# Kernel tuning notes

Measured on AMD Instinct MI355X. Metric: run time of the kernel, lower is better.

The kernel has to match this reference:

```python
import jax, jax.numpy as jnp
import numpy as np

H, DK, DV, S = 16, 1024, 1024, 2048
DH_QK = DK // H  # 64, per-head q/k dim
DH_V = DV // H   # 64, per-head v dim


def setup_inputs() -> dict:
    key = jax.random.key(0)
    ks = jax.random.split(key, 11)
    init = lambda k, shape, fan_in: jax.random.uniform(k, shape, jnp.float32, -1.0, 1.0) / jnp.sqrt(jnp.float32(fan_in))
    return {
        "Q": jax.random.normal(ks[0], (S, DK), jnp.float32),
        "K": jax.random.normal(ks[1], (S, DK), jnp.float32),
        "V": jax.random.normal(ks[2], (S, DV), jnp.float32),
        # per-head Linear weights, torch convention [out, in] stacked over heads
        "Wq": init(ks[3], (H, DH_QK, DH_QK), DH_QK),
        "bq": init(ks[4], (H, DH_QK), DH_QK),
        "Wk": init(ks[5], (H, DH_QK, DH_QK), DH_QK),
        "bk": init(ks[6], (H, DH_QK), DH_QK),
        "Wv": init(ks[7], (H, DH_V, DH_V), DH_V),
        "bv": init(ks[8], (H, DH_V), DH_V),
        "Wo": init(ks[9], (DK, H * DH_V), H * DH_V),  # final linear: d_model x (h*dv_h)
        "bo": init(ks[10], (DK,), H * DH_V),
    }


def reference(Q, K, V, Wq, bq, Wk, bk, Wv, bv, Wo, bo):
    h, dh = Wq.shape[0], Wq.shape[2]
    dv = Wv.shape[2]
    s = Q.shape[0]
    # split features into h per-head chunks (same as slicing loop in torch)
    Qh = Q.reshape(s, h, dh)
    Kh = K.reshape(s, h, dh)
    Vh = V.reshape(s, h, dv)
    # per-head Linear: x @ W.T + b, batched over heads
    q = jnp.einsum('shd,hed->she', Qh, Wq) + bq
    k = jnp.einsum('shd,hed->she', Kh, Wk) + bk
    v = jnp.einsum('shd,hed->she', Vh, Wv) + bv
    # scaled dot-product attention per head
    scores = jnp.einsum('she,the->hst', q, k) / jnp.sqrt(jnp.float32(dh))
    attn = jax.nn.softmax(scores, axis=-1)
    o = jnp.einsum('hst,the->she', attn, v)  # [s, h, dv]
    concat = o.reshape(s, h * dv)
    return concat @ Wo.T + bo
```

## Files before the change

kernel.cpp:

```cpp
#include <hip/hip_runtime.h>
#include <stdint.h>

static constexpr int H   = 16;
static constexpr int S   = 2048;
static constexpr int DHd = 64;
static constexpr int DM  = 1024;
static constexpr int NSPLIT = 4;
static constexpr int KT_PER_SPLIT = (S / 64) / NSPLIT;

using f32x4   = __attribute__((ext_vector_type(4))) float;
using f32x8   = __attribute__((ext_vector_type(8))) float;
using f32x16  = __attribute__((ext_vector_type(16))) float;
using short8  = __attribute__((ext_vector_type(8))) short;
using bf16x8  = __attribute__((ext_vector_type(8))) __bf16;
using uint4v  = __attribute__((ext_vector_type(4))) unsigned int;

#if __has_builtin(__builtin_amdgcn_exp2f)
#define EXP2F __builtin_amdgcn_exp2f
#else
#define EXP2F exp2f
#endif

__device__ __forceinline__ short f2bf(float f) {
  union { float f; uint32_t u; } v; v.f = f;
  uint32_t r = v.u + 0x7FFFu + ((v.u >> 16) & 1u);
  return (short)(r >> 16);
}
__device__ __forceinline__ float bf2f(short s) {
  union { uint32_t u; float f; } v;
  v.u = ((uint32_t)(unsigned short)s) << 16;
  return v.f;
}

__device__ __forceinline__ short8 f2bf8(f32x4 a, f32x4 b) {
  short8 v;
  v[0] = f2bf(a[0]); v[1] = f2bf(a[1]); v[2] = f2bf(a[2]); v[3] = f2bf(a[3]);
  v[4] = f2bf(b[0]); v[5] = f2bf(b[1]); v[6] = f2bf(b[2]); v[7] = f2bf(b[3]);
  return v;
}

__device__ __forceinline__ unsigned int pkbf(float a, float b) {
  __bf16 x = (__bf16)a, y = (__bf16)b;
  unsigned short ux = __builtin_bit_cast(unsigned short, x);
  unsigned short uy = __builtin_bit_cast(unsigned short, y);
  return (unsigned int)ux | ((unsigned int)uy << 16);
}

__device__ __forceinline__ f32x4 mfma16(short8 a, short8 b, f32x4 c) {
  return __builtin_amdgcn_mfma_f32_16x16x32_bf16(
      __builtin_bit_cast(bf16x8, a), __builtin_bit_cast(bf16x8, b), c, 0, 0, 0);
}
__device__ __forceinline__ f32x16 mfma32(short8 a, short8 b, f32x16 c) {
  return __builtin_amdgcn_mfma_f32_32x32x16_bf16(
      __builtin_bit_cast(bf16x8, a), __builtin_bit_cast(bf16x8, b), c, 0, 0, 0);
}

__device__ __forceinline__ short8 lds_read_swz(const short* base, int row, int chunk) {
  return *(const short8*)((const char*)base + row * 128 + ((chunk ^ (row & 7)) << 4));
}
__device__ __forceinline__ void lds_write_swz(short* base, int row, int chunk, short8 v) {
  *(short8*)((char*)base + row * 128 + ((chunk ^ (row & 7)) << 4)) = v;
}

using u32g = __attribute__((address_space(1))) const unsigned int;
using u32l = __attribute__((address_space(3))) unsigned int;
__device__ __forceinline__ void gl_lds16(const short* g, short* l) {
  __builtin_amdgcn_global_load_lds(
      reinterpret_cast<u32g*>(reinterpret_cast<uintptr_t>(g)),
      reinterpret_cast<u32l*>(static_cast<unsigned int>(reinterpret_cast<uintptr_t>(l))),
      16, 0, 0);
}

__global__ __launch_bounds__(256) void proj_kernel(
    const float* __restrict__ Q, const float* __restrict__ K, const float* __restrict__ V,
    const float* __restrict__ Wq, const float* __restrict__ bq,
    const float* __restrict__ Wk, const float* __restrict__ bk,
    const float* __restrict__ Wv, const float* __restrict__ bv,
    const float* __restrict__ Wo, short* __restrict__ wob,
    short* __restrict__ qb, short* __restrict__ kb, short* __restrict__ vtb) {
  const int t = threadIdx.x;
  const int mode = blockIdx.z;

  if (mode == 3) {
    int chunk = blockIdx.y * gridDim.x + blockIdx.x;
    int i = (chunk * 256 + t) * 16;
    f32x4 x0 = *(const f32x4*)(Wo + i);
    f32x4 x1 = *(const f32x4*)(Wo + i + 4);
    f32x4 x2 = *(const f32x4*)(Wo + i + 8);
    f32x4 x3 = *(const f32x4*)(Wo + i + 12);
    *(short8*)(wob + i)     = f2bf8(x0, x1);
    *(short8*)(wob + i + 8) = f2bf8(x2, x3);
    return;
  }

  const int h  = blockIdx.y;
  const int rt = blockIdx.x * 128;

  const float* X; const float* W; const float* bias;
  if (mode == 0)      { X = Q; W = Wq; bias = bq; }
  else if (mode == 1) { X = K; W = Wk; bias = bk; }
  else                { X = V; W = Wv; bias = bv; }
  bias += h * DHd;
  const float scale = (mode == 0) ? 0.125f * 1.44269504f : 1.0f;

  __shared__ short Xs[128 * 64];
  __shared__ short Ws[64 * 64];
  __shared__ short Ot[64 * 136];

#pragma unroll
  for (int p = 0; p < 4; p++) {
    int ci = p * 256 + t;
    int row = ci >> 3, oct = ci & 7;
    const float* g = X + (size_t)(rt + row) * DM + h * DHd + oct * 8;
    f32x4 x0 = *(const f32x4*)g;
    f32x4 x1 = *(const f32x4*)(g + 4);
    lds_write_swz(Xs, row, oct, f2bf8(x0, x1));
  }
#pragma unroll
  for (int p = 0; p < 2; p++) {
    int ci = p * 256 + t;
    int row = ci >> 3, oct = ci & 7;
    const float* g = W + (size_t)h * DHd * DHd + row * DHd + oct * 8;
    f32x4 x0 = *(const f32x4*)g;
    f32x4 x1 = *(const f32x4*)(g + 4);
    lds_write_swz(Ws, row, oct, f2bf8(x0, x1));
  }
  __syncthreads();

  const int wid = t >> 6, lane = t & 63;
  const int l15 = lane & 15, l4 = lane >> 4;

  f32x4 acc[2][4] = {};
#pragma unroll
  for (int ks = 0; ks < 2; ks++) {
    int chunk = ks * 4 + l4;
    short8 a0 = lds_read_swz(Xs, wid * 32 + l15, chunk);
    short8 a1 = lds_read_swz(Xs, wid * 32 + 16 + l15, chunk);
#pragma unroll
    for (int nf = 0; nf < 4; nf++) {
      short8 b = lds_read_swz(Ws, nf * 16 + l15, chunk);
      acc[0][nf] = mfma16(a0, b, acc[0][nf]);
      acc[1][nf] = mfma16(a1, b, acc[1][nf]);
    }
  }

  if (mode < 2) {
    short* out = (mode == 0) ? qb : kb;
#pragma unroll
    for (int mf = 0; mf < 2; mf++)
#pragma unroll
      for (int nf = 0; nf < 4; nf++) {
        int col = nf * 16 + l15;
        float b = bias[col];
#pragma unroll
        for (int r = 0; r < 4; r++) {
          int row = rt + wid * 32 + mf * 16 + l4 * 4 + r;
          out[((size_t)h * S + row) * DHd + col] = f2bf((acc[mf][nf][r] + b) * scale);
        }
      }
  } else {
#pragma unroll
    for (int mf = 0; mf < 2; mf++)
#pragma unroll
      for (int nf = 0; nf < 4; nf++) {
        int col = nf * 16 + l15;
        float b = bias[col];
#pragma unroll
        for (int r = 0; r < 4; r++) {
          int lrow = wid * 32 + mf * 16 + l4 * 4 + r;
          Ot[col * 136 + lrow] = f2bf(acc[mf][nf][r] + b);
        }
      }
    __syncthreads();
#pragma unroll
    for (int p = 0; p < 2; p++) {
      int ci = p * 256 + t;
      int e = ci >> 3, c16 = ci & 7;
      short8 a = *(const short8*)&Ot[e * 136 + c16 * 16];
      short8 b = *(const short8*)&Ot[e * 136 + c16 * 16 + 8];
      short8 lo, hi;
      lo[0] = a[0]; lo[1] = a[1]; lo[2] = a[2]; lo[3] = a[3];
      lo[4] = b[0]; lo[5] = b[1]; lo[6] = b[2]; lo[7] = b[3];
      hi[0] = a[4]; hi[1] = a[5]; hi[2] = a[6]; hi[3] = a[7];
      hi[4] = b[4]; hi[5] = b[5]; hi[6] = b[6]; hi[7] = b[7];
      short* dst = vtb + ((size_t)h * DHd + e) * S + rt + c16 * 16;
      *(short8*)dst       = lo;
      *(short8*)(dst + 8) = hi;
    }
  }
}

__global__ __launch_bounds__(256, 2) void attn_kernel(
    const short* __restrict__ qb, const short* __restrict__ kb,
    const short* __restrict__ vtb, short* __restrict__ OpT,
    float* __restrict__ lbuf) {
  const int h  = blockIdx.y;
  const int sp = blockIdx.z;
  const int t = threadIdx.x, wid = t >> 6, lane = t & 63;
  const int l31 = lane & 31, l5 = lane >> 5;
  const int qw = blockIdx.x * 256 + wid * 64;

  __shared__ short Ks[2][64 * 64];
  __shared__ short Vs[2][64 * 64];

  short8 qf[2][4];
#pragma unroll
  for (int tt = 0; tt < 2; tt++) {
    const short* qrow = qb + ((size_t)h * S + qw + tt * 32 + l31) * DHd;
#pragma unroll
    for (int c = 0; c < 4; c++) qf[tt][c] = *(const short8*)(qrow + c * 16 + l5 * 8);
  }

  const int srow8 = lane >> 3, schunk = lane & 7;
  const int r0 = wid * 16 + srow8, r1 = r0 + 8;
  const int kt0 = sp * KT_PER_SPLIT;
  const short* kg0 = kb + ((size_t)h * S + (size_t)kt0 * 64 + r0) * DHd + ((schunk ^ (r0 & 7)) * 8);
  const short* kg1 = kb + ((size_t)h * S + (size_t)kt0 * 64 + r1) * DHd + ((schunk ^ (r1 & 7)) * 8);
  const short* vg0 = vtb + ((size_t)h * DHd + r0) * S + (size_t)kt0 * 64 + ((schunk ^ (r0 & 7)) * 8);
  const short* vg1 = vtb + ((size_t)h * DHd + r1) * S + (size_t)kt0 * 64 + ((schunk ^ (r1 & 7)) * 8);

  auto stage = [&](int buf, int kk) {
    const size_t ka = (size_t)kk * 64 * DHd;
    const size_t va = (size_t)kk * 64;
    gl_lds16(kg0 + ka, &Ks[buf][wid * 1024]);
    gl_lds16(kg1 + ka, &Ks[buf][wid * 1024 + 512]);
    gl_lds16(vg0 + va, &Vs[buf][wid * 1024]);
    gl_lds16(vg1 + va, &Vs[buf][wid * 1024 + 512]);
  };

  stage(0, 0);
  asm volatile("s_waitcnt vmcnt(0)" ::: "memory");
  __syncthreads();

  f32x16 oa00 = {}, oa01 = {}, oa10 = {}, oa11 = {};
  f32x8 lac0 = {}, lac1 = {};

  for (int kk = 0; kk < KT_PER_SPLIT; kk++) {
    const int cur = kk & 1;
    if (kk + 1 < KT_PER_SPLIT) stage(cur ^ 1, kk + 1);

    f32x16 s00 = {}, s01 = {}, s10 = {}, s11 = {};
    __builtin_amdgcn_s_setprio(1);
#pragma unroll
    for (int c = 0; c < 4; c++) {
      short8 ak0 = lds_read_swz(Ks[cur], l31, 2 * c + l5);
      short8 ak1 = lds_read_swz(Ks[cur], 32 + l31, 2 * c + l5);
      s00 = mfma32(ak0, qf[0][c], s00);
      s01 = mfma32(ak1, qf[0][c], s01);
      s10 = mfma32(ak0, qf[1][c], s10);
      s11 = mfma32(ak1, qf[1][c], s11);
    }
    __builtin_amdgcn_s_setprio(0);

#pragma unroll
    for (int i = 0; i < 16; i++) {
      float p00 = EXP2F(s00[i]), p01 = EXP2F(s01[i]);
      float p10 = EXP2F(s10[i]), p11 = EXP2F(s11[i]);
      s00[i] = p00; s01[i] = p01; s10[i] = p10; s11[i] = p11;
      lac0[i & 7] += p00 + p01;
      lac1[i & 7] += p10 + p11;
    }

    unsigned int pk0[2][8], pk1[2][8];
#pragma unroll
    for (int g = 0; g < 4; g++) {
      pk0[0][g * 2 + 0] = pkbf(s00[4 * g + 0], s00[4 * g + 1]);
      pk0[0][g * 2 + 1] = pkbf(s00[4 * g + 2], s00[4 * g + 3]);
      pk0[1][g * 2 + 0] = pkbf(s01[4 * g + 0], s01[4 * g + 1]);
      pk0[1][g * 2 + 1] = pkbf(s01[4 * g + 2], s01[4 * g + 3]);
      pk1[0][g * 2 + 0] = pkbf(s10[4 * g + 0], s10[4 * g + 1]);
      pk1[0][g * 2 + 1] = pkbf(s10[4 * g + 2], s10[4 * g + 3]);
      pk1[1][g * 2 + 0] = pkbf(s11[4 * g + 0], s11[4 * g + 1]);
      pk1[1][g * 2 + 1] = pkbf(s11[4 * g + 2], s11[4 * g + 3]);
    }

    __builtin_amdgcn_s_setprio(1);
#pragma unroll
    for (int j = 0; j < 4; j++) {
      const int bb = j >> 1;
      const int s4 = (j & 1) * 4;
      short8 av0 = lds_read_swz(Vs[cur], l31, 2 * j + l5);
      short8 av1 = lds_read_swz(Vs[cur], 32 + l31, 2 * j + l5);
      uint4v pf0, pf1;
      pf0[0] = pk0[bb][s4 + 0]; pf0[1] = pk0[bb][s4 + 1];
      pf0[2] = pk0[bb][s4 + 2]; pf0[3] = pk0[bb][s4 + 3];
      pf1[0] = pk1[bb][s4 + 0]; pf1[1] = pk1[bb][s4 + 1];
      pf1[2] = pk1[bb][s4 + 2]; pf1[3] = pk1[bb][s4 + 3];
      short8 p0 = __builtin_bit_cast(short8, pf0);
      short8 p1 = __builtin_bit_cast(short8, pf1);
      oa00 = mfma32(av0, p0, oa00);
      oa01 = mfma32(av1, p0, oa01);
      oa10 = mfma32(av0, p1, oa10);
      oa11 = mfma32(av1, p1, oa11);
    }
    __builtin_amdgcn_s_setprio(0);

    asm volatile("s_waitcnt vmcnt(0)" ::: "memory");
    __syncthreads();
  }

#pragma unroll
  for (int st = 4; st >= 1; st >>= 1)
#pragma unroll
    for (int i = 0; i < st; i++) { lac0[i] += lac0[i + st]; lac1[i] += lac1[i + st]; }
  float l0 = lac0[0] + __shfl_xor(lac0[0], 32);
  float l1 = lac1[0] + __shfl_xor(lac1[0], 32);

#pragma unroll
  for (int r = 0; r < 16; r++) {
    int dvb = (r & 3) + 8 * (r >> 2) + 4 * l5;
    size_t base = (((size_t)sp * H + h) * DHd + dvb) * S + qw + l31;
    OpT[base]            = f2bf(oa00[r]);
    OpT[base + 32UL * S] = f2bf(oa01[r]);
    OpT[base + 32]            = f2bf(oa10[r]);
    OpT[base + 32UL * S + 32] = f2bf(oa11[r]);
  }
  if (l5 == 0) {
    lbuf[((size_t)sp * H + h) * S + qw + l31]      = l0;
    lbuf[((size_t)sp * H + h) * S + qw + 32 + l31] = l1;
  }
}

__global__ __launch_bounds__(256) void combine_kernel(
    const short* __restrict__ OpT, const float* __restrict__ lbuf,
    short* __restrict__ Ob) {
  const int h  = blockIdx.y;
  const int s0 = blockIdx.x * 64;
  __shared__ short tile[64][72];

  const int t = threadIdx.x;
  const int sl = t & 63, dvg = t >> 6;
  const int s = s0 + sl;

  float lt = 0.f;
#pragma unroll
  for (int sp = 0; sp < NSPLIT; sp++)
    lt += lbuf[((size_t)sp * H + h) * S + s];
  float inv = 1.0f / lt;

  float val[16];
#pragma unroll
  for (int p = 0; p < 16; p++) {
    int dv = dvg * 16 + p;
    float o = 0.f;
#pragma unroll
    for (int sp = 0; sp < NSPLIT; sp++)
      o += bf2f(OpT[(((size_t)sp * H + h) * DHd + dv) * S + s]);
    val[p] = o * inv;
  }
  short8 v0, v1;
#pragma unroll
  for (int i = 0; i < 8; i++) { v0[i] = f2bf(val[i]); v1[i] = f2bf(val[8 + i]); }
  *(short8*)&tile[sl][dvg * 16]     = v0;
  *(short8*)&tile[sl][dvg * 16 + 8] = v1;
  __syncthreads();

#pragma unroll
  for (int i = 0; i < 2; i++) {
    int cid = t + i * 256;
    int r = cid >> 3, c = cid & 7;
    short8 v = *(const short8*)&tile[r][c * 8];
    *(short8*)(Ob + (size_t)(s0 + r) * DM + h * DHd + c * 8) = v;
  }
}

__global__ __launch_bounds__(256) void out_gemm(
    const short* __restrict__ Ob, const short* __restrict__ wob,
    const float* __restrict__ bo, float* __restrict__ out) {
  const int m0 = blockIdx.x * 64;
  const int n0 = blockIdx.y * 64;

  __shared__ short As[2][64 * 64];
  __shared__ short Bs[2][64 * 64];

  const int t = threadIdx.x, wid = t >> 6, lane = t & 63;
  const int l15 = lane & 15, l4 = lane >> 4;
  const int srow8 = lane >> 3, schunk = lane & 7;
  const int r0 = wid * 16 + srow8, r1 = r0 + 8;

  const short* ag0 = Ob  + (size_t)(m0 + r0) * DM + ((schunk ^ (r0 & 7)) * 8);
  const short* ag1 = Ob  + (size_t)(m0 + r1) * DM + ((schunk ^ (r1 & 7)) * 8);
  const short* bg0 = wob + (size_t)(n0 + r0) * DM + ((schunk ^ (r0 & 7)) * 8);
  const short* bg1 = wob + (size_t)(n0 + r1) * DM + ((schunk ^ (r1 & 7)) * 8);

  auto stage = [&](int buf, int kc) {
    const int off = kc * 64;
    gl_lds16(ag0 + off, &As[buf][wid * 1024]);
    gl_lds16(ag1 + off, &As[buf][wid * 1024 + 512]);
    gl_lds16(bg0 + off, &Bs[buf][wid * 1024]);
    gl_lds16(bg1 + off, &Bs[buf][wid * 1024 + 512]);
  };

  stage(0, 0);
  asm volatile("s_waitcnt vmcnt(0)" ::: "memory");
  __syncthreads();

  f32x4 acc[4] = {};
  for (int kc = 0; kc < DM / 64; kc++) {
    const int cur = kc & 1;
    if (kc + 1 < DM / 64) stage(cur ^ 1, kc + 1);
#pragma unroll
    for (int ks = 0; ks < 2; ks++) {
      int chunk = ks * 4 + l4;
      short8 a = lds_read_swz(As[cur], wid * 16 + l15, chunk);
#pragma unroll
      for (int nf = 0; nf < 4; nf++) {
        short8 b = lds_read_swz(Bs[cur], nf * 16 + l15, chunk);
        acc[nf] = mfma16(a, b, acc[nf]);
      }
    }
    asm volatile("s_waitcnt vmcnt(0)" ::: "memory");
    __syncthreads();
  }
#pragma unroll
  for (int nf = 0; nf < 4; nf++) {
    int col = n0 + nf * 16 + l15;
    float b = bo[col];
#pragma unroll
    for (int r = 0; r < 4; r++) {
      int row = m0 + wid * 16 + l4 * 4 + r;
      out[(size_t)row * DM + col] = acc[nf][r] + b;
    }
  }
}

extern "C" void kernel_launch(void* const* d_in, const int* in_sizes, int n_in,
                              void* d_out, int out_size, void* d_ws, size_t ws_size,
                              hipStream_t stream) {
  const float* Q  = (const float*)d_in[0];
  const float* K  = (const float*)d_in[1];
  const float* V  = (const float*)d_in[2];
  const float* Wq = (const float*)d_in[3];
  const float* bq = (const float*)d_in[4];
  const float* Wk = (const float*)d_in[5];
  const float* bk = (const float*)d_in[6];
  const float* Wv = (const float*)d_in[7];
  const float* bv = (const float*)d_in[8];
  const float* Wo = (const float*)d_in[9];
  const float* bo = (const float*)d_in[10];

  char* ws = (char*)d_ws;
  short* qb   = (short*)(ws);
  short* kb   = (short*)(ws + ((size_t)4 << 20));
  short* vtb  = (short*)(ws + ((size_t)8 << 20));
  short* Obf  = (short*)(ws + ((size_t)12 << 20));
  short* wob  = (short*)(ws + ((size_t)16 << 20));
  short* OpT  = (short*)(ws + ((size_t)18 << 20));
  float* lbuf = (float*)(ws + ((size_t)34 << 20));

  proj_kernel<<<dim3(S / 128, H, 4), 256, 0, stream>>>(Q, K, V, Wq, bq, Wk, bk, Wv, bv,
                                                       Wo, wob, qb, kb, vtb);
  attn_kernel<<<dim3(S / 256, H, NSPLIT), 256, 0, stream>>>(qb, kb, vtb, OpT, lbuf);
  combine_kernel<<<dim3(S / 64, H), 256, 0, stream>>>(OpT, lbuf, Obf);
  out_gemm<<<dim3(S / 64, DM / 64), 256, 0, stream>>>(Obf, wob, bo, (float*)d_out);
}
```

Before: 52.09 us.

## Triple-buffer K/V and GEMM tiles with single barrier per iteration; reorder attn grid

The attention and output GEMM loops go from double to triple buffering of LDS tiles. Each loop keeps two tile loads in flight, waits only for the oldest with a partial vmcnt, and needs one barrier per iteration instead of a full drain at the end. The attention grid is also reordered so head and split vary fastest, which may change L2 reuse of K/V across concurrently scheduled blocks. LDS use grows by half, which could lower occupancy, and the vmcnt(4) count relies on each stage issuing exactly four global-to-LDS loads.

Measured after the change: 52.01 us. About the same (-0.2%).

```diff
diff --git a/kernel.cpp b/kernel.cpp
--- a/kernel.cpp
+++ b/kernel.cpp
@@ -194,14 +194,14 @@
     const short* __restrict__ qb, const short* __restrict__ kb,
     const short* __restrict__ vtb, short* __restrict__ OpT,
     float* __restrict__ lbuf) {
-  const int h  = blockIdx.y;
-  const int sp = blockIdx.z;
+  const int h  = blockIdx.x;
+  const int sp = blockIdx.y;
   const int t = threadIdx.x, wid = t >> 6, lane = t & 63;
   const int l31 = lane & 31, l5 = lane >> 5;
-  const int qw = blockIdx.x * 256 + wid * 64;
-
-  __shared__ short Ks[2][64 * 64];
-  __shared__ short Vs[2][64 * 64];
+  const int qw = blockIdx.z * 256 + wid * 64;
+
+  __shared__ short Ks[3][64 * 64];
+  __shared__ short Vs[3][64 * 64];
 
   short8 qf[2][4];
 #pragma unroll
@@ -229,15 +229,17 @@
   };
 
   stage(0, 0);
-  asm volatile("s_waitcnt vmcnt(0)" ::: "memory");
-  __syncthreads();
+  stage(1, 1);
 
   f32x16 oa00 = {}, oa01 = {}, oa10 = {}, oa11 = {};
   f32x8 lac0 = {}, lac1 = {};
 
   for (int kk = 0; kk < KT_PER_SPLIT; kk++) {
-    const int cur = kk & 1;
-    if (kk + 1 < KT_PER_SPLIT) stage(cur ^ 1, kk + 1);
+    const int cur = kk % 3;
+    if (kk + 1 < KT_PER_SPLIT) asm volatile("s_waitcnt vmcnt(4)" ::: "memory");
+    else                       asm volatile("s_waitcnt vmcnt(0)" ::: "memory");
+    __syncthreads();
+    if (kk + 2 < KT_PER_SPLIT) stage((kk + 2) % 3, kk + 2);
 
     f32x16 s00 = {}, s01 = {}, s10 = {}, s11 = {};
     __builtin_amdgcn_s_setprio(1);
@@ -294,9 +296,6 @@
       oa11 = mfma32(av1, p1, oa11);
     }
     __builtin_amdgcn_s_setprio(0);
-
-    asm volatile("s_waitcnt vmcnt(0)" ::: "memory");
-    __syncthreads();
   }
 
 #pragma unroll
@@ -369,9 +368,10 @@
     const float* __restrict__ bo, float* __restrict__ out) {
   const int m0 = blockIdx.x * 64;
   const int n0 = blockIdx.y * 64;
-
-  __shared__ short As[2][64 * 64];
-  __shared__ short Bs[2][64 * 64];
+  constexpr int KT = DM / 64;
+
+  __shared__ short As[3][64 * 64];
+  __shared__ short Bs[3][64 * 64];
 
   const int t = threadIdx.x, wid = t >> 6, lane = t & 63;
   const int l15 = lane & 15, l4 = lane >> 4;
@@ -392,13 +392,15 @@
   };
 
   stage(0, 0);
-  asm volatile("s_waitcnt vmcnt(0)" ::: "memory");
-  __syncthreads();
+  stage(1, 1);
 
   f32x4 acc[4] = {};
-  for (int kc = 0; kc < DM / 64; kc++) {
-    const int cur = kc & 1;
-    if (kc + 1 < DM / 64) stage(cur ^ 1, kc + 1);
+  for (int kc = 0; kc < KT; kc++) {
+    const int cur = kc % 3;
+    if (kc + 1 < KT) asm volatile("s_waitcnt vmcnt(4)" ::: "memory");
+    else             asm volatile("s_waitcnt vmcnt(0)" ::: "memory");
+    __syncthreads();
+    if (kc + 2 < KT) stage((kc + 2) % 3, kc + 2);
 #pragma unroll
     for (int ks = 0; ks < 2; ks++) {
       int chunk = ks * 4 + l4;
@@ -409,8 +411,6 @@
         acc[nf] = mfma16(a, b, acc[nf]);
       }
     }
-    asm volatile("s_waitcnt vmcnt(0)" ::: "memory");
-    __syncthreads();
   }
 #pragma unroll
   for (int nf = 0; nf < 4; nf++) {
@@ -450,7 +450,7 @@
 
   proj_kernel<<<dim3(S / 128, H, 4), 256, 0, stream>>>(Q, K, V, Wq, bq, Wk, bk, Wv, bv,
                                                        Wo, wob, qb, kb, vtb);
-  attn_kernel<<<dim3(S / 256, H, NSPLIT), 256, 0, stream>>>(qb, kb, vtb, OpT, lbuf);
+  attn_kernel<<<dim3(H, NSPLIT, S / 256), 256, 0, stream>>>(qb, kb, vtb, OpT, lbuf);
   combine_kernel<<<dim3(S / 64, H), 256, 0, stream>>>(OpT, lbuf, Obf);
   out_gemm<<<dim3(S / 64, DM / 64), 256, 0, stream>>>(Obf, wob, bo, (float*)d_out);
 }
```
